# Kernel tuning notes

Measured on AMD Instinct MI355X. Metric: run time of the kernel, lower is better.

The kernel has to match this reference:

```python
import jax, jax.numpy as jnp
import numpy as np

L_XYZ = 10  # fourier freqs for position -> 3 + 6*10 = 63 dims
L_DIR = 4   # fourier freqs for direction -> 3 + 6*4 = 27 dims
DIM = 32    # radiance feature dim per depth layer
PPP = 4     # points (depth layers) per pixel
HID = 128   # MLP hidden width
UCH = 64    # UNet hidden channels


def pe(x, L):
    # fourier positional encoding: [x, sin(2^k x), cos(2^k x)]
    f = (2.0 ** jnp.arange(L)).astype(x.dtype)
    xf = x[..., None] * f  # [..., 3, L]
    s = jnp.sin(xf).reshape(x.shape[:-1] + (-1,))
    c = jnp.cos(xf).reshape(x.shape[:-1] + (-1,))
    return jnp.concatenate([x, s, c], axis=-1)


def conv(x, w, b):
    y = jax.lax.conv_general_dilated(x, w, (1, 1), 'SAME',
                                     dimension_numbers=('NCHW', 'OIHW', 'NCHW'))
    return y + b[None, :, None, None]


def setup_inputs() -> dict:
    key = jax.random.key(0)
    ks = jax.random.split(key, 24)
    H = W = 384
    zbufs = jax.random.uniform(ks[0], (H, W, PPP), dtype=jnp.float32)  # depths in [0,1)
    o = jax.random.normal(ks[1], (H, W, 3), dtype=jnp.float32)
    d = jax.random.normal(ks[2], (H, W, 3), dtype=jnp.float32)
    d = d / jnp.linalg.norm(d, axis=-1, keepdims=True)
    cos = jax.random.uniform(ks[3], (H, W, 1), dtype=jnp.float32) * 0.5 + 0.5
    ray = jnp.concatenate([o, d, cos], axis=-1)  # [H,W,7]
    gt = jax.random.uniform(ks[4], (H, W, 3), dtype=jnp.float32)
    mask_gt = jnp.ones((H, W, 1), dtype=jnp.float32)
    xyz_o = jax.random.normal(ks[5], (1024, 3), dtype=jnp.float32)
    in_xyz = 3 + 6 * L_XYZ
    in_dir = 3 + 6 * L_DIR
    in_ch = DIM * PPP
    p = {}
    p['w1'] = jax.random.normal(ks[6], (in_xyz, HID), dtype=jnp.float32) * 0.05
    p['b1'] = jnp.zeros((HID,), dtype=jnp.float32)
    p['w2'] = jax.random.normal(ks[7], (HID, HID), dtype=jnp.float32) * 0.05
    p['b2'] = jnp.zeros((HID,), dtype=jnp.float32)
    p['w3'] = jax.random.normal(ks[8], (HID + in_dir, DIM), dtype=jnp.float32) * 0.05
    p['b3'] = jnp.zeros((DIM,), dtype=jnp.float32)
    p['mpn_w1'] = jax.random.normal(ks[9], (in_ch, in_ch, 3, 3), dtype=jnp.float32) * 0.02
    p['mpn_b1'] = jnp.zeros((in_ch,), dtype=jnp.float32)
    p['mpn_w2'] = jax.random.normal(ks[10], (in_ch, in_ch, 3, 3), dtype=jnp.float32) * 0.02
    p['mpn_b2'] = jnp.zeros((in_ch,), dtype=jnp.float32)
    p['uw1'] = jax.random.normal(ks[11], (UCH, in_ch, 3, 3), dtype=jnp.float32) * 0.02
    p['ub1'] = jnp.zeros((UCH,), dtype=jnp.float32)
    p['uw2'] = jax.random.normal(ks[12], (UCH, UCH, 3, 3), dtype=jnp.float32) * 0.02
    p['ub2'] = jnp.zeros((UCH,), dtype=jnp.float32)
    p['uw3'] = jax.random.normal(ks[13], (3, UCH, 3, 3), dtype=jnp.float32) * 0.02
    p['ub3'] = jnp.zeros((3,), dtype=jnp.float32)
    inp = {'zbufs': zbufs, 'ray': ray, 'gt': gt, 'mask_gt': mask_gt,
           'isTrain': 1, 'xyz_o': xyz_o}
    inp.update(p)
    return inp


def reference(zbufs, ray, gt, mask_gt, isTrain, xyz_o,
              w1, b1, w2, b2, w3, b3,
              mpn_w1, mpn_b1, mpn_w2, mpn_b2,
              uw1, ub1, uw2, ub2, uw3, ub3):
    H, W, P = zbufs.shape
    o = ray[..., :3]
    dirs = ray[..., 3:6]
    cos = ray[..., 6:7]
    thresh = 0.2 if isTrain else 0.0
    # dense equivalent of boolean-mask gather -> MLP -> scatter into zeros
    mask = (zbufs > thresh).astype(zbufs.dtype)  # [H,W,P]
    # xyz_near = o + dirs * zbuf / cos  (xyznear path)
    xyz = o[..., None, :] + dirs[..., None, :] * zbufs[..., None] / cos[..., None]  # [H,W,P,3]
    x = pe(xyz, L_XYZ)                                   # [H,W,P,63]
    h = jax.nn.relu(x @ w1 + b1)                         # [H,W,P,HID]
    h = jax.nn.relu(h @ w2 + b2)
    dpe = pe(dirs, L_DIR)                                # [H,W,27]
    dpe = jnp.broadcast_to(dpe[..., None, :], h.shape[:-1] + (dpe.shape[-1],))
    feat = jnp.concatenate([h, dpe], axis=-1) @ w3 + b3  # [H,W,P,DIM]
    feat = feat * mask[..., None]                        # zeros where pix_mask is False
    # per-layer permute(2,3,0,1) + cat(dim=1) == [1, P*DIM, H, W]
    rdmp = feat.transpose(2, 3, 0, 1).reshape(1, P * DIM, H, W)
    # MPN: predicted per-channel mask
    m = jax.nn.sigmoid(conv(jax.nn.relu(conv(rdmp, mpn_w1, mpn_b1)), mpn_w2, mpn_b2))
    fuse = rdmp * m
    fea_map = jax.nn.sigmoid(fuse[0, :3].transpose(1, 2, 0))  # [H,W,3]
    # UNet refinement to RGB
    u = jax.nn.relu(conv(fuse, uw1, ub1))
    u = jax.nn.relu(conv(u, uw2, ub2))
    img = jax.nn.sigmoid(conv(u, uw3, ub3))[0].transpose(1, 2, 0)  # [H,W,3]
    return img
```

## Files before the change

kernel.cpp:

```cpp
#include <hip/hip_runtime.h>
#include <hip/hip_bf16.h>
#include <math.h>

typedef __attribute__((ext_vector_type(8))) unsigned short ushort8;
typedef __attribute__((ext_vector_type(8))) __bf16 bf16x8;
typedef __attribute__((ext_vector_type(4))) float floatx4;

constexpr int IMGW = 384;
constexpr int NPIX = IMGW * IMGW;

__device__ __forceinline__ unsigned short f2bf(float f) {
  union { float f; unsigned u; } v; v.f = f;
  unsigned u = v.u;
  return (unsigned short)((u + 0x7fffu + ((u >> 16) & 1u)) >> 16);
}
__device__ __forceinline__ float bf2f(unsigned short h) {
  union { unsigned u; float f; } v; v.u = ((unsigned)h) << 16; return v.f;
}
__device__ __forceinline__ unsigned pk2bf(float a, float b) {
  float2 f2; f2.x = a; f2.y = b;
  __hip_bfloat162 h = __float22bfloat162_rn(f2);
  union { __hip_bfloat162 h; unsigned u; } u; u.h = h; return u.u;
}
__device__ __forceinline__ unsigned short cvt1bf(float a) {
  return (unsigned short)pk2bf(a, a);
}
__device__ __forceinline__ floatx4 mfma16(bf16x8 a, bf16x8 b, floatx4 c) {
  return __builtin_amdgcn_mfma_f32_16x16x32_bf16(a, b, c, 0, 0, 0);
}
__device__ __forceinline__ bf16x8 lds_frag(const unsigned short* p) {
  return *reinterpret_cast<const bf16x8*>(p);
}

__global__ void prep_mlpA(const float* __restrict__ w1, const float* __restrict__ w2,
                          const float* __restrict__ w3,
                          unsigned short* __restrict__ w1A, unsigned short* __restrict__ w2A,
                          unsigned short* __restrict__ w3A) {
  int i = blockIdx.x * 256 + threadIdx.x;
  if (i < 8192) {
    int j = i & 7, lane = (i >> 3) & 63, t = i >> 9;
    int mt = t >> 1, ks = t & 1;
    int ch = mt * 16 + (lane & 15), k = ks * 32 + (lane >> 4) * 8 + j;
    w1A[i] = f2bf(k < 63 ? w1[k * 128 + ch] : 0.0f);
  } else if (i < 24576) {
    int i2 = i - 8192;
    int j = i2 & 7, lane = (i2 >> 3) & 63, t = i2 >> 9;
    int mt = t >> 2, ks = t & 3;
    int ch = mt * 16 + (lane & 15), k = ks * 32 + (lane >> 4) * 8 + j;
    w2A[i2] = f2bf(w2[k * 128 + ch]);
  } else if (i < 28672) {
    int i3 = i - 24576;
    int j = i3 & 7, lane = (i3 >> 3) & 63, t = i3 >> 9;
    int mt = t >> 2, ks = t & 3;
    int ch = mt * 16 + (lane & 15), k = ks * 32 + (lane >> 4) * 8 + j;
    w3A[i3] = f2bf(w3[k * 32 + ch]);
  }
}

__global__ void prep_convB(const float* __restrict__ w, unsigned short* __restrict__ wt,
                           int total, int CIN, int G, int NT) {
  int i = blockIdx.x * 256 + threadIdx.x;
  if (i >= total) return;
  int j = i & 7, lane = (i >> 3) & 63;
  int rest = i >> 9;
  int nt = rest % NT; int rest2 = rest / NT;
  int g = rest2 % G;  int ks = rest2 / G;
  int q = lane >> 4, m = lane & 15;
  int co = (g * NT + nt) * 16 + m;
  int k = ks * 32 + q * 8 + j;
  int nb = k / CIN, ci = k - nb * CIN;
  wt[i] = f2bf(w[(co * CIN + ci) * 9 + nb]);
}

__global__ __launch_bounds__(256) void dcon_kernel(
    const float* __restrict__ ray, const float* __restrict__ w3,
    const float* __restrict__ b3, float* __restrict__ dconG) {
  int gid = blockIdx.x * 256 + threadIdx.x;
  int pixel = gid >> 5, c = gid & 31;
  const float* r = ray + (size_t)pixel * 7;
  float d0 = r[3], d1 = r[4], d2 = r[5];
  float acc = b3[c];
  acc += d0 * w3[128 * 32 + c] + d1 * w3[129 * 32 + c] + d2 * w3[130 * 32 + c];
  float dv[3] = { d0, d1, d2 };
  #pragma unroll
  for (int cc = 0; cc < 3; ++cc) {
    float fs = 1.0f;
    #pragma unroll
    for (int f = 0; f < 4; ++f) {
      float s, co;
      __sincosf(dv[cc] * fs, &s, &co);
      acc += s * w3[(131 + cc * 4 + f) * 32 + c];
      acc += co * w3[(143 + cc * 4 + f) * 32 + c];
      fs *= 2.0f;
    }
  }
  dconG[gid] = acc;
}

__global__ __launch_bounds__(128, 4) void mlp_kernel(
    const float* __restrict__ zbufs, const float* __restrict__ ray,
    const int* __restrict__ isTrain,
    const float* __restrict__ b1, const float* __restrict__ b2,
    const unsigned short* __restrict__ w1A, const unsigned short* __restrict__ w2A,
    const unsigned short* __restrict__ w3A, const float* __restrict__ dconG,
    unsigned short* __restrict__ rdmp) {
  __shared__ __align__(16) unsigned short H[64 * 136];

  const int tid = threadIdx.x;
  const int wave = tid >> 6, lane = tid & 63, q = lane >> 4, m = lane & 15;
  const int s0 = wave * 32;
  const float thresh = (isTrain[0] != 0) ? 0.2f : 0.0f;

  {
    int s = s0 + (lane >> 1), h = lane & 1;
    int sg = blockIdx.x * 64 + s;
    int pixel = sg >> 2;
    float z = zbufs[sg];
    const float* r = ray + (size_t)pixel * 7;
    float t = z / r[6];
    float xv[3] = { r[0] + r[3] * t, r[1] + r[4] * t, r[2] + r[5] * t };
    unsigned short* Xr = H + s * 136;
    if (h == 0) {
      Xr[0] = cvt1bf(xv[0]); Xr[1] = cvt1bf(xv[1]); Xr[2] = cvt1bf(xv[2]);
      Xr[63] = 0;
    }
    float fb = h ? 32.0f : 1.0f;
    int fo = h * 5;
    #pragma unroll
    for (int c = 0; c < 3; ++c) {
      float s_, c_;
      __sincosf(xv[c] * fb, &s_, &c_);
      #pragma unroll
      for (int fi = 0; fi < 5; ++fi) {
        Xr[3 + c * 10 + fo + fi]  = cvt1bf(s_);
        Xr[33 + c * 10 + fo + fi] = cvt1bf(c_);
        float t2 = s_ + s_;
        float ns = t2 * c_;
        float nc = fmaf(-t2, s_, 1.0f);
        s_ = ns; c_ = nc;
      }
    }
  }

  {
    floatx4 acc[8][2] = {};
    #pragma unroll 1
    for (int ks = 0; ks < 2; ++ks) {
      bf16x8 a[8];
      #pragma unroll
      for (int mt = 0; mt < 8; ++mt)
        a[mt] = *reinterpret_cast<const bf16x8*>(w1A + (((mt << 1) + ks) << 9) + lane * 8);
      bf16x8 bf[2];
      #pragma unroll
      for (int nt = 0; nt < 2; ++nt)
        bf[nt] = lds_frag(H + (s0 + nt * 16 + m) * 136 + ks * 32 + q * 8);
      #pragma unroll
      for (int mt = 0; mt < 8; ++mt)
        #pragma unroll
        for (int nt = 0; nt < 2; ++nt)
          acc[mt][nt] = mfma16(a[mt], bf[nt], acc[mt][nt]);
    }
    #pragma unroll
    for (int mt = 0; mt < 8; ++mt) {
      float4 bb = *reinterpret_cast<const float4*>(b1 + mt * 16 + q * 4);
      #pragma unroll
      for (int nt = 0; nt < 2; ++nt) {
        float v0 = fmaxf(acc[mt][nt][0] + bb.x, 0.0f);
        float v1 = fmaxf(acc[mt][nt][1] + bb.y, 0.0f);
        float v2 = fmaxf(acc[mt][nt][2] + bb.z, 0.0f);
        float v3 = fmaxf(acc[mt][nt][3] + bb.w, 0.0f);
        uint2 pk; pk.x = pk2bf(v0, v1); pk.y = pk2bf(v2, v3);
        *reinterpret_cast<uint2*>(&H[(s0 + nt * 16 + m) * 136 + mt * 16 + q * 4]) = pk;
      }
    }
  }

  {
    floatx4 acc[8][2] = {};
    #pragma unroll 1
    for (int ks = 0; ks < 4; ++ks) {
      bf16x8 a[8];
      #pragma unroll
      for (int mt = 0; mt < 8; ++mt)
        a[mt] = *reinterpret_cast<const bf16x8*>(w2A + (((mt << 2) + ks) << 9) + lane * 8);
      bf16x8 bf[2];
      #pragma unroll
      for (int nt = 0; nt < 2; ++nt)
        bf[nt] = lds_frag(H + (s0 + nt * 16 + m) * 136 + ks * 32 + q * 8);
      #pragma unroll
      for (int mt = 0; mt < 8; ++mt)
        #pragma unroll
        for (int nt = 0; nt < 2; ++nt)
          acc[mt][nt] = mfma16(a[mt], bf[nt], acc[mt][nt]);
    }
    #pragma unroll
    for (int mt = 0; mt < 8; ++mt) {
      float4 bb = *reinterpret_cast<const float4*>(b2 + mt * 16 + q * 4);
      #pragma unroll
      for (int nt = 0; nt < 2; ++nt) {
        float v0 = fmaxf(acc[mt][nt][0] + bb.x, 0.0f);
        float v1 = fmaxf(acc[mt][nt][1] + bb.y, 0.0f);
        float v2 = fmaxf(acc[mt][nt][2] + bb.z, 0.0f);
        float v3 = fmaxf(acc[mt][nt][3] + bb.w, 0.0f);
        uint2 pk; pk.x = pk2bf(v0, v1); pk.y = pk2bf(v2, v3);
        *reinterpret_cast<uint2*>(&H[(s0 + nt * 16 + m) * 136 + mt * 16 + q * 4]) = pk;
      }
    }
  }

  {
    floatx4 acc[2][2];
    const float* dg = dconG + (size_t)blockIdx.x * 512;
    #pragma unroll
    for (int nt = 0; nt < 2; ++nt) {
      int s = s0 + nt * 16 + m;
      #pragma unroll
      for (int mt = 0; mt < 2; ++mt)
        acc[mt][nt] = *reinterpret_cast<const floatx4*>(dg + (s >> 2) * 32 + mt * 16 + q * 4);
    }
    #pragma unroll 1
    for (int ks = 0; ks < 4; ++ks) {
      bf16x8 a[2];
      #pragma unroll
      for (int mt = 0; mt < 2; ++mt)
        a[mt] = *reinterpret_cast<const bf16x8*>(w3A + (((mt << 2) + ks) << 9) + lane * 8);
      bf16x8 bf[2];
      #pragma unroll
      for (int nt = 0; nt < 2; ++nt)
        bf[nt] = lds_frag(H + (s0 + nt * 16 + m) * 136 + ks * 32 + q * 8);
      #pragma unroll
      for (int mt = 0; mt < 2; ++mt)
        #pragma unroll
        for (int nt = 0; nt < 2; ++nt)
          acc[mt][nt] = mfma16(a[mt], bf[nt], acc[mt][nt]);
    }
    #pragma unroll
    for (int nt = 0; nt < 2; ++nt) {
      int s = s0 + nt * 16 + m;
      float z = zbufs[blockIdx.x * 64 + s];
      float mk = (z > thresh) ? 1.0f : 0.0f;
      unsigned short* dst = rdmp + (size_t)blockIdx.x * 2048 + s * 32 + q * 4;
      #pragma unroll
      for (int mt = 0; mt < 2; ++mt) {
        uint2 pk;
        pk.x = pk2bf(acc[mt][nt][0] * mk, acc[mt][nt][1] * mk);
        pk.y = pk2bf(acc[mt][nt][2] * mk, acc[mt][nt][3] * mk);
        *reinterpret_cast<uint2*>(dst + mt * 16) = pk;
      }
    }
  }
}

template<int CIN, int COUT, int WAVES, int MODE>
__global__ __launch_bounds__(WAVES * 64, 3) void conv3x3(
    const unsigned short* __restrict__ in, const unsigned short* __restrict__ wt,
    const float* __restrict__ bias, const unsigned short* __restrict__ rdmp,
    unsigned short* __restrict__ out) {
  constexpr int CP  = CIN + 8;
  constexpr int CH8 = CIN / 8;
  constexpr int KC  = CIN / 32;
  constexpr int NT  = COUT / (WAVES * 16);
  __shared__ __align__(16) unsigned short lds_in[6 * 18 * CP];

  const int tid = threadIdx.x;
  const int x0 = blockIdx.x * 16, y0 = blockIdx.y * 4;

  for (int i = tid; i < 108 * CH8; i += WAVES * 64) {
    int pix = i / CH8, part = i - pix * CH8;
    int xx = pix % 18, yy = pix / 18;
    int gx = x0 - 1 + xx, gy = y0 - 1 + yy;
    ushort8 v = {0, 0, 0, 0, 0, 0, 0, 0};
    if (gx >= 0 && gx < IMGW && gy >= 0 && gy < IMGW)
      v = *reinterpret_cast<const ushort8*>(in + ((size_t)(gy * IMGW + gx)) * CIN + part * 8);
    *reinterpret_cast<ushort8*>(&lds_in[pix * CP + part * 8]) = v;
  }
  __syncthreads();

  const int wave = tid >> 6, lane = tid & 63, q = lane >> 4, m = lane & 15;
  floatx4 acc[4][NT] = {};

  #pragma unroll 1
  for (int kc = 0; kc < KC; ++kc) {
    bf16x8 a[6][3];
    #pragma unroll
    for (int rr = 0; rr < 6; ++rr)
      #pragma unroll
      for (int dx = 0; dx < 3; ++dx)
        a[rr][dx] = lds_frag(&lds_in[(rr * 18 + m + dx) * CP + kc * 32 + q * 8]);
    #pragma unroll
    for (int nb = 0; nb < 9; ++nb) {
      int dy = nb / 3, dx = nb - dy * 3;
      int ks = nb * KC + kc;
      #pragma unroll
      for (int nt = 0; nt < NT; ++nt) {
        bf16x8 b = *reinterpret_cast<const bf16x8*>(
            wt + ((((size_t)ks * WAVES + wave) * NT + nt) << 9) + lane * 8);
        #pragma unroll
        for (int mt = 0; mt < 4; ++mt)
          acc[mt][nt] = mfma16(a[mt + dy][dx], b, acc[mt][nt]);
      }
    }
  }

  const int co0 = wave * (COUT / WAVES);
  #pragma unroll
  for (int mt = 0; mt < 4; ++mt) {
    int y = y0 + mt;
    #pragma unroll
    for (int nt = 0; nt < NT; ++nt) {
      int co = co0 + nt * 16 + m;
      float bb = bias[co];
      #pragma unroll
      for (int r = 0; r < 4; ++r) {
        int pixel = y * IMGW + x0 + q * 4 + r;
        float v = acc[mt][nt][r] + bb;
        if (MODE == 0) {
          v = fmaxf(v, 0.0f);
        } else {
          v = 1.0f / (1.0f + __expf(-v));
          v *= bf2f(rdmp[(size_t)pixel * 128 + co]);
        }
        out[(size_t)pixel * COUT + co] = f2bf(v);
      }
    }
  }
}

__global__ __launch_bounds__(256) void uconv3_kernel(
    const unsigned short* __restrict__ u2, const float* __restrict__ w,
    const float* __restrict__ b, float* __restrict__ out) {
  __shared__ float wl[1728];
  for (int i = threadIdx.x; i < 1728; i += 256) {
    int c = i % 3; int t = i / 3; int ci = t & 63; int nb = t >> 6;
    wl[i] = w[(c * 64 + ci) * 9 + nb];
  }
  __syncthreads();
  int pixel = blockIdx.x * 256 + threadIdx.x;
  int py = pixel / IMGW, px = pixel - py * IMGW;
  float a0 = b[0], a1 = b[1], a2 = b[2];
  for (int nb = 0; nb < 9; ++nb) {
    int gy = py + nb / 3 - 1, gx = px + nb % 3 - 1;
    if (gx < 0 || gx >= IMGW || gy < 0 || gy >= IMGW) continue;
    const unsigned short* src = u2 + (size_t)(gy * IMGW + gx) * 64;
    const float* wp = wl + nb * 192;
    #pragma unroll
    for (int cc = 0; cc < 8; ++cc) {
      ushort8 v = *reinterpret_cast<const ushort8*>(src + cc * 8);
      #pragma unroll
      for (int j = 0; j < 8; ++j) {
        float uv = bf2f(v[j]);
        const float* w3p = wp + (cc * 8 + j) * 3;
        a0 += uv * w3p[0]; a1 += uv * w3p[1]; a2 += uv * w3p[2];
      }
    }
  }
  float* o = out + (size_t)pixel * 3;
  o[0] = 1.0f / (1.0f + __expf(-a0));
  o[1] = 1.0f / (1.0f + __expf(-a1));
  o[2] = 1.0f / (1.0f + __expf(-a2));
}

extern "C" void kernel_launch(void* const* d_in, const int* in_sizes, int n_in,
                              void* d_out, int out_size, void* d_ws, size_t ws_size,
                              hipStream_t stream) {
  (void)in_sizes; (void)n_in; (void)out_size; (void)ws_size;
  const float* zbufs = (const float*)d_in[0];
  const float* ray   = (const float*)d_in[1];
  const int* isTrain = (const int*)d_in[4];
  const float* w1 = (const float*)d_in[6];
  const float* b1 = (const float*)d_in[7];
  const float* w2 = (const float*)d_in[8];
  const float* b2 = (const float*)d_in[9];
  const float* w3 = (const float*)d_in[10];
  const float* b3 = (const float*)d_in[11];
  const float* mpn_w1 = (const float*)d_in[12];
  const float* mpn_b1 = (const float*)d_in[13];
  const float* mpn_w2 = (const float*)d_in[14];
  const float* mpn_b2 = (const float*)d_in[15];
  const float* uw1 = (const float*)d_in[16];
  const float* ub1 = (const float*)d_in[17];
  const float* uw2 = (const float*)d_in[18];
  const float* ub2 = (const float*)d_in[19];
  const float* uw3 = (const float*)d_in[20];
  const float* ub3 = (const float*)d_in[21];
  float* out = (float*)d_out;

  unsigned char* ws = (unsigned char*)d_ws;
  size_t off = 0;
  auto alloc = [&](size_t bytes) -> void* {
    void* p = ws + off; off = (off + bytes + 255) & ~(size_t)255; return p;
  };
  unsigned short* w1A  = (unsigned short*)alloc(8192 * 2);
  unsigned short* w2A  = (unsigned short*)alloc(16384 * 2);
  unsigned short* w3A  = (unsigned short*)alloc(4096 * 2);
  unsigned short* cw1  = (unsigned short*)alloc((size_t)128 * 1152 * 2);
  unsigned short* cw2  = (unsigned short*)alloc((size_t)128 * 1152 * 2);
  unsigned short* cu1  = (unsigned short*)alloc((size_t)64 * 1152 * 2);
  unsigned short* cu2  = (unsigned short*)alloc((size_t)64 * 576 * 2);
  unsigned short* rdmp = (unsigned short*)alloc((size_t)NPIX * 128 * 2);
  unsigned short* t1   = (unsigned short*)alloc((size_t)NPIX * 128 * 2);
  unsigned short* fuse = (unsigned short*)alloc((size_t)NPIX * 128 * 2);
  unsigned short* u1 = t1;
  unsigned short* u2 = rdmp;
  float* dconG = (float*)fuse;

  prep_mlpA<<<112, 256, 0, stream>>>(w1, w2, w3, w1A, w2A, w3A);
  prep_convB<<<576, 256, 0, stream>>>(mpn_w1, cw1, 128 * 1152, 128, 4, 2);
  prep_convB<<<576, 256, 0, stream>>>(mpn_w2, cw2, 128 * 1152, 128, 4, 2);
  prep_convB<<<288, 256, 0, stream>>>(uw1, cu1, 64 * 1152, 128, 2, 2);
  prep_convB<<<144, 256, 0, stream>>>(uw2, cu2, 64 * 576, 64, 2, 2);

  dcon_kernel<<<NPIX * 32 / 256, 256, 0, stream>>>(ray, w3, b3, dconG);
  mlp_kernel<<<NPIX * 4 / 64, 128, 0, stream>>>(zbufs, ray, isTrain, b1, b2,
                                                w1A, w2A, w3A, dconG, rdmp);

  dim3 cgrid(IMGW / 16, IMGW / 4);
  conv3x3<128, 128, 4, 0><<<cgrid, 256, 0, stream>>>(rdmp, cw1, mpn_b1, nullptr, t1);
  conv3x3<128, 128, 4, 1><<<cgrid, 256, 0, stream>>>(t1, cw2, mpn_b2, rdmp, fuse);
  conv3x3<128, 64, 2, 0><<<cgrid, 128, 0, stream>>>(fuse, cu1, ub1, nullptr, u1);
  conv3x3<64, 64, 2, 0><<<cgrid, 128, 0, stream>>>(u1, cu2, ub2, nullptr, u2);
  uconv3_kernel<<<NPIX / 256, 256, 0, stream>>>(u2, uw3, ub3, out);
}
```

Measured before the change: 365.3 us.

## Build MLP positional-encoding fragments in registers and permute weight K layouts

The positional encoding for the first MLP layer is now computed directly into MFMA B-operand registers, with the w1 K-dimension permuted so each lane's 8-element fragment comes from two sincos calls plus one doubling step. This removes the LDS staging of the encoding. The w2/w3 K orderings are permuted so the hidden activations can be written to LDS with 16-byte stores instead of 8-byte ones. Biases are folded into the accumulator initialisation, z is reused for the mask instead of reloaded, and loops are unrolled with per-tile weight loads. Launch bounds occupancy drops from 4 to 3, trading occupancy for more registers.

```diff
diff --git a/kernel.cpp b/kernel.cpp
--- a/kernel.cpp
+++ b/kernel.cpp
@@ -22,14 +22,14 @@
   __hip_bfloat162 h = __float22bfloat162_rn(f2);
   union { __hip_bfloat162 h; unsigned u; } u; u.h = h; return u.u;
 }
-__device__ __forceinline__ unsigned short cvt1bf(float a) {
-  return (unsigned short)pk2bf(a, a);
-}
 __device__ __forceinline__ floatx4 mfma16(bf16x8 a, bf16x8 b, floatx4 c) {
   return __builtin_amdgcn_mfma_f32_16x16x32_bf16(a, b, c, 0, 0, 0);
 }
 __device__ __forceinline__ bf16x8 lds_frag(const unsigned short* p) {
   return *reinterpret_cast<const bf16x8*>(p);
+}
+__device__ __forceinline__ bf16x8 u4_to_bf(uint4 v) {
+  union { uint4 u; bf16x8 b; } c; c.u = v; return c.b;
 }
 
 __global__ void prep_mlpA(const float* __restrict__ w1, const float* __restrict__ w2,
@@ -40,20 +40,40 @@
   if (i < 8192) {
     int j = i & 7, lane = (i >> 3) & 63, t = i >> 9;
     int mt = t >> 1, ks = t & 1;
-    int ch = mt * 16 + (lane & 15), k = ks * 32 + (lane >> 4) * 8 + j;
-    w1A[i] = f2bf(k < 63 ? w1[k * 128 + ch] : 0.0f);
+    int ch_out = mt * 16 + (lane & 15);
+    int kp = ks * 32 + (lane >> 4) * 8 + j;
+    int chunk = kp >> 3, sl = kp & 7;
+    float val;
+    if (chunk == 7 && sl >= 4) {
+      int c = sl - 4;
+      val = (c < 3) ? w1[c * 128 + ch_out] : 0.0f;
+    } else {
+      const int coordA[8] = {0,0,0,1,1,2,2,2};
+      const int octA[8]   = {0,4,8,2,6,0,4,8};
+      const int coordB[8] = {0,0,1,1,1,2,2,2};
+      const int octB[8]   = {2,6,0,4,8,2,6,0};
+      int rc  = (sl < 4) ? coordA[chunk] : coordB[chunk];
+      int oct = ((sl < 4) ? octA[chunk] : octB[chunk]) + ((sl >> 1) & 1);
+      int korig = ((sl & 1) ? 33 : 3) + rc * 10 + oct;
+      val = w1[korig * 128 + ch_out];
+    }
+    w1A[i] = f2bf(val);
   } else if (i < 24576) {
     int i2 = i - 8192;
     int j = i2 & 7, lane = (i2 >> 3) & 63, t = i2 >> 9;
     int mt = t >> 2, ks = t & 3;
-    int ch = mt * 16 + (lane & 15), k = ks * 32 + (lane >> 4) * 8 + j;
-    w2A[i2] = f2bf(w2[k * 128 + ch]);
+    int ch_out = mt * 16 + (lane & 15);
+    int kp = ks * 32 + (lane >> 4) * 8 + j;
+    int c_orig = ((kp >> 2) & 7) * 16 + (kp >> 5) * 4 + (kp & 3);
+    w2A[i2] = f2bf(w2[c_orig * 128 + ch_out]);
   } else if (i < 28672) {
     int i3 = i - 24576;
     int j = i3 & 7, lane = (i3 >> 3) & 63, t = i3 >> 9;
     int mt = t >> 2, ks = t & 3;
-    int ch = mt * 16 + (lane & 15), k = ks * 32 + (lane >> 4) * 8 + j;
-    w3A[i3] = f2bf(w3[k * 32 + ch]);
+    int ch_out = mt * 16 + (lane & 15);
+    int kp = ks * 32 + (lane >> 4) * 8 + j;
+    int c_orig = ((kp >> 2) & 7) * 16 + (kp >> 5) * 4 + (kp & 3);
+    w3A[i3] = f2bf(w3[c_orig * 32 + ch_out]);
   }
 }
 
@@ -97,7 +117,7 @@
   dconG[gid] = acc;
 }
 
-__global__ __launch_bounds__(128, 4) void mlp_kernel(
+__global__ __launch_bounds__(128, 3) void mlp_kernel(
     const float* __restrict__ zbufs, const float* __restrict__ ray,
     const int* __restrict__ isTrain,
     const float* __restrict__ b1, const float* __restrict__ b2,
@@ -111,99 +131,126 @@
   const int s0 = wave * 32;
   const float thresh = (isTrain[0] != 0) ? 0.2f : 0.0f;
 
-  {
-    int s = s0 + (lane >> 1), h = lane & 1;
+  float fA[2], fB[2];
+  int cAi[2], cBi[2];
+  #pragma unroll
+  for (int half = 0; half < 2; ++half) {
+    int ch = half * 4 + q;
+    cAi[half] = (ch <= 2) ? 0 : ((ch <= 4) ? 1 : 2);
+    fA[half]  = (ch == 0 || ch == 5) ? 1.0f :
+                (ch == 1 || ch == 6) ? 16.0f :
+                (ch == 2 || ch == 7) ? 256.0f :
+                (ch == 3) ? 4.0f : 64.0f;
+    cBi[half] = (ch <= 1) ? 0 : ((ch <= 4) ? 1 : 2);
+    fB[half]  = (ch == 2) ? 1.0f :
+                (ch == 0 || ch == 5) ? 4.0f :
+                (ch == 3) ? 16.0f :
+                (ch == 1 || ch == 6) ? 64.0f : 256.0f;
+  }
+
+  bf16x8 bx[2][2];
+  float zs[2];
+  #pragma unroll
+  for (int nt = 0; nt < 2; ++nt) {
+    int s = s0 + nt * 16 + m;
     int sg = blockIdx.x * 64 + s;
     int pixel = sg >> 2;
     float z = zbufs[sg];
+    zs[nt] = z;
     const float* r = ray + (size_t)pixel * 7;
     float t = z / r[6];
-    float xv[3] = { r[0] + r[3] * t, r[1] + r[4] * t, r[2] + r[5] * t };
-    unsigned short* Xr = H + s * 136;
-    if (h == 0) {
-      Xr[0] = cvt1bf(xv[0]); Xr[1] = cvt1bf(xv[1]); Xr[2] = cvt1bf(xv[2]);
-      Xr[63] = 0;
-    }
-    float fb = h ? 32.0f : 1.0f;
-    int fo = h * 5;
-    #pragma unroll
-    for (int c = 0; c < 3; ++c) {
-      float s_, c_;
-      __sincosf(xv[c] * fb, &s_, &c_);
-      #pragma unroll
-      for (int fi = 0; fi < 5; ++fi) {
-        Xr[3 + c * 10 + fo + fi]  = cvt1bf(s_);
-        Xr[33 + c * 10 + fo + fi] = cvt1bf(c_);
-        float t2 = s_ + s_;
-        float ns = t2 * c_;
-        float nc = fmaf(-t2, s_, 1.0f);
-        s_ = ns; c_ = nc;
-      }
+    float xv0 = r[0] + r[3] * t, xv1 = r[1] + r[4] * t, xv2 = r[2] + r[5] * t;
+    #pragma unroll
+    for (int half = 0; half < 2; ++half) {
+      float uA = (cAi[half] == 0) ? xv0 : ((cAi[half] == 1) ? xv1 : xv2);
+      float uB = (cBi[half] == 0) ? xv0 : ((cBi[half] == 1) ? xv1 : xv2);
+      float sa, ca, sb, cb;
+      __sincosf(uA * fA[half], &sa, &ca);
+      __sincosf(uB * fB[half], &sb, &cb);
+      float t2a = sa + sa;
+      float sa1 = t2a * ca, ca1 = fmaf(-t2a, sa, 1.0f);
+      float t2b = sb + sb;
+      float sb1 = t2b * cb, cb1 = fmaf(-t2b, sb, 1.0f);
+      if (half == 1 && q == 3) { sb = xv0; cb = xv1; sb1 = xv2; cb1 = 0.0f; }
+      uint4 dv;
+      dv.x = pk2bf(sa, ca); dv.y = pk2bf(sa1, ca1);
+      dv.z = pk2bf(sb, cb); dv.w = pk2bf(sb1, cb1);
+      bx[nt][half] = u4_to_bf(dv);
     }
   }
 
   {
-    floatx4 acc[8][2] = {};
-    #pragma unroll 1
+    floatx4 acc[8][2];
+    #pragma unroll
+    for (int mt = 0; mt < 8; ++mt) {
+      float4 bb = *reinterpret_cast<const float4*>(b1 + mt * 16 + q * 4);
+      #pragma unroll
+      for (int nt = 0; nt < 2; ++nt) {
+        acc[mt][nt][0] = bb.x; acc[mt][nt][1] = bb.y;
+        acc[mt][nt][2] = bb.z; acc[mt][nt][3] = bb.w;
+      }
+    }
+    #pragma unroll
     for (int ks = 0; ks < 2; ++ks) {
-      bf16x8 a[8];
-      #pragma unroll
-      for (int mt = 0; mt < 8; ++mt)
-        a[mt] = *reinterpret_cast<const bf16x8*>(w1A + (((mt << 1) + ks) << 9) + lane * 8);
+      #pragma unroll
+      for (int mt = 0; mt < 8; ++mt) {
+        bf16x8 a = *reinterpret_cast<const bf16x8*>(w1A + (((mt << 1) + ks) << 9) + lane * 8);
+        #pragma unroll
+        for (int nt = 0; nt < 2; ++nt)
+          acc[mt][nt] = mfma16(a, bx[nt][ks], acc[mt][nt]);
+      }
+    }
+    #pragma unroll
+    for (int nt = 0; nt < 2; ++nt) {
+      uint4* base = reinterpret_cast<uint4*>(&H[(s0 + nt * 16 + m) * 136 + q * 32]);
+      #pragma unroll
+      for (int g = 0; g < 4; ++g) {
+        uint4 v;
+        v.x = pk2bf(fmaxf(acc[2*g][nt][0], 0.0f),   fmaxf(acc[2*g][nt][1], 0.0f));
+        v.y = pk2bf(fmaxf(acc[2*g][nt][2], 0.0f),   fmaxf(acc[2*g][nt][3], 0.0f));
+        v.z = pk2bf(fmaxf(acc[2*g+1][nt][0], 0.0f), fmaxf(acc[2*g+1][nt][1], 0.0f));
+        v.w = pk2bf(fmaxf(acc[2*g+1][nt][2], 0.0f), fmaxf(acc[2*g+1][nt][3], 0.0f));
+        base[g] = v;
+      }
+    }
+  }
+
+  {
+    floatx4 acc[8][2];
+    #pragma unroll
+    for (int mt = 0; mt < 8; ++mt) {
+      float4 bb = *reinterpret_cast<const float4*>(b2 + mt * 16 + q * 4);
+      #pragma unroll
+      for (int nt = 0; nt < 2; ++nt) {
+        acc[mt][nt][0] = bb.x; acc[mt][nt][1] = bb.y;
+        acc[mt][nt][2] = bb.z; acc[mt][nt][3] = bb.w;
+      }
+    }
+    #pragma unroll 2
+    for (int ks = 0; ks < 4; ++ks) {
       bf16x8 bf[2];
       #pragma unroll
       for (int nt = 0; nt < 2; ++nt)
         bf[nt] = lds_frag(H + (s0 + nt * 16 + m) * 136 + ks * 32 + q * 8);
       #pragma unroll
-      for (int mt = 0; mt < 8; ++mt)
+      for (int mt = 0; mt < 8; ++mt) {
+        bf16x8 a = *reinterpret_cast<const bf16x8*>(w2A + (((mt << 2) + ks) << 9) + lane * 8);
         #pragma unroll
         for (int nt = 0; nt < 2; ++nt)
-          acc[mt][nt] = mfma16(a[mt], bf[nt], acc[mt][nt]);
-    }
-    #pragma unroll
-    for (int mt = 0; mt < 8; ++mt) {
-      float4 bb = *reinterpret_cast<const float4*>(b1 + mt * 16 + q * 4);
-      #pragma unroll
-      for (int nt = 0; nt < 2; ++nt) {
-        float v0 = fmaxf(acc[mt][nt][0] + bb.x, 0.0f);
-        float v1 = fmaxf(acc[mt][nt][1] + bb.y, 0.0f);
-        float v2 = fmaxf(acc[mt][nt][2] + bb.z, 0.0f);
-        float v3 = fmaxf(acc[mt][nt][3] + bb.w, 0.0f);
-        uint2 pk; pk.x = pk2bf(v0, v1); pk.y = pk2bf(v2, v3);
-        *reinterpret_cast<uint2*>(&H[(s0 + nt * 16 + m) * 136 + mt * 16 + q * 4]) = pk;
-      }
-    }
-  }
-
-  {
-    floatx4 acc[8][2] = {};
-    #pragma unroll 1
-    for (int ks = 0; ks < 4; ++ks) {
-      bf16x8 a[8];
-      #pragma unroll
-      for (int mt = 0; mt < 8; ++mt)
-        a[mt] = *reinterpret_cast<const bf16x8*>(w2A + (((mt << 2) + ks) << 9) + lane * 8);
-      bf16x8 bf[2];
-      #pragma unroll
-      for (int nt = 0; nt < 2; ++nt)
-        bf[nt] = lds_frag(H + (s0 + nt * 16 + m) * 136 + ks * 32 + q * 8);
-      #pragma unroll
-      for (int mt = 0; mt < 8; ++mt)
-        #pragma unroll
-        for (int nt = 0; nt < 2; ++nt)
-          acc[mt][nt] = mfma16(a[mt], bf[nt], acc[mt][nt]);
-    }
-    #pragma unroll
-    for (int mt = 0; mt < 8; ++mt) {
-      float4 bb = *reinterpret_cast<const float4*>(b2 + mt * 16 + q * 4);
-      #pragma unroll
-      for (int nt = 0; nt < 2; ++nt) {
-        float v0 = fmaxf(acc[mt][nt][0] + bb.x, 0.0f);
-        float v1 = fmaxf(acc[mt][nt][1] + bb.y, 0.0f);
-        float v2 = fmaxf(acc[mt][nt][2] + bb.z, 0.0f);
-        float v3 = fmaxf(acc[mt][nt][3] + bb.w, 0.0f);
-        uint2 pk; pk.x = pk2bf(v0, v1); pk.y = pk2bf(v2, v3);
-        *reinterpret_cast<uint2*>(&H[(s0 + nt * 16 + m) * 136 + mt * 16 + q * 4]) = pk;
+          acc[mt][nt] = mfma16(a, bf[nt], acc[mt][nt]);
+      }
+    }
+    #pragma unroll
+    for (int nt = 0; nt < 2; ++nt) {
+      uint4* base = reinterpret_cast<uint4*>(&H[(s0 + nt * 16 + m) * 136 + q * 32]);
+      #pragma unroll
+      for (int g = 0; g < 4; ++g) {
+        uint4 v;
+        v.x = pk2bf(fmaxf(acc[2*g][nt][0], 0.0f),   fmaxf(acc[2*g][nt][1], 0.0f));
+        v.y = pk2bf(fmaxf(acc[2*g][nt][2], 0.0f),   fmaxf(acc[2*g][nt][3], 0.0f));
+        v.z = pk2bf(fmaxf(acc[2*g+1][nt][0], 0.0f), fmaxf(acc[2*g+1][nt][1], 0.0f));
+        v.w = pk2bf(fmaxf(acc[2*g+1][nt][2], 0.0f), fmaxf(acc[2*g+1][nt][3], 0.0f));
+        base[g] = v;
       }
     }
   }
@@ -218,27 +265,24 @@
       for (int mt = 0; mt < 2; ++mt)
         acc[mt][nt] = *reinterpret_cast<const floatx4*>(dg + (s >> 2) * 32 + mt * 16 + q * 4);
     }
-    #pragma unroll 1
+    #pragma unroll 2
     for (int ks = 0; ks < 4; ++ks) {
-      bf16x8 a[2];
-      #pragma unroll
-      for (int mt = 0; mt < 2; ++mt)
-        a[mt] = *reinterpret_cast<const bf16x8*>(w3A + (((mt << 2) + ks) << 9) + lane * 8);
       bf16x8 bf[2];
       #pragma unroll
       for (int nt = 0; nt < 2; ++nt)
         bf[nt] = lds_frag(H + (s0 + nt * 16 + m) * 136 + ks * 32 + q * 8);
       #pragma unroll
-      for (int mt = 0; mt < 2; ++mt)
+      for (int mt = 0; mt < 2; ++mt) {
+        bf16x8 a = *reinterpret_cast<const bf16x8*>(w3A + (((mt << 2) + ks) << 9) + lane * 8);
         #pragma unroll
         for (int nt = 0; nt < 2; ++nt)
-          acc[mt][nt] = mfma16(a[mt], bf[nt], acc[mt][nt]);
+          acc[mt][nt] = mfma16(a, bf[nt], acc[mt][nt]);
+      }
     }
     #pragma unroll
     for (int nt = 0; nt < 2; ++nt) {
       int s = s0 + nt * 16 + m;
-      float z = zbufs[blockIdx.x * 64 + s];
-      float mk = (z > thresh) ? 1.0f : 0.0f;
+      float mk = (zs[nt] > thresh) ? 1.0f : 0.0f;
       unsigned short* dst = rdmp + (size_t)blockIdx.x * 2048 + s * 32 + q * 4;
       #pragma unroll
       for (int mt = 0; mt < 2; ++mt) {
```

After: 368.4 us. No clear change (+0.9%).
